# Optimization experiments

Measured on AMD Instinct MI355X. Metric: run time of the kernel, lower is better.

The kernel has to match this reference:

```python
import jax, jax.numpy as jnp
import numpy as np

N_NODES = 100000
D_FEAT = 64
E1 = 1600000  # 1-hop edges (avg degree 16)
E2 = 6400000  # 2-hop edges (avg degree 64)


def setup_inputs() -> dict:
    key = jax.random.key(0)
    k_x, k_ei1, k_w1, k_ei2, k_w2 = jax.random.split(key, 5)
    x = jax.random.normal(k_x, (N_NODES, D_FEAT), dtype=jnp.float32)
    edge_index1 = jax.random.randint(k_ei1, (2, E1), 0, N_NODES, dtype=jnp.int32)
    edge_weight1 = jax.random.uniform(k_w1, (E1,), dtype=jnp.float32)
    edge_index2 = jax.random.randint(k_ei2, (2, E2), 0, N_NODES, dtype=jnp.int32)
    edge_weight2 = jax.random.uniform(k_w2, (E2,), dtype=jnp.float32)
    return {
        "x": x,
        "edge_index1": edge_index1,
        "edge_weight1": edge_weight1,
        "edge_index2": edge_index2,
        "edge_weight2": edge_weight2,
    }


def _spmm(edge_index, edge_weight, x, num_nodes):
    # out[i] = sum_{(i,j) in E} w_ij * x[j]   (COO SpMM via gather + segment_sum)
    dst, src = edge_index[0], edge_index[1]
    msgs = edge_weight[:, None] * x[src]            # [E, d] gather + scale
    return jax.ops.segment_sum(msgs, dst, num_segments=num_nodes)  # [N, d]


def reference(x, edge_index1, edge_weight1, edge_index2, edge_weight2):
    n = x.shape[0]
    x1 = _spmm(edge_index1, edge_weight1, x, n)  # adj_t @ x
    x2 = _spmm(edge_index2, edge_weight2, x, n)  # adj_t2 @ x
    return jnp.concatenate([x1, x2], axis=1)     # [N, 2d]
```

## Files before the change

### kernel.cpp

```cpp
#include <hip/hip_runtime.h>
#include <hip/hip_bf16.h>

#define D 64
#define RB 8
#define RSZ 256
#define MAXB 1024
#define CH 4096
#define SCT 1024
#define GCH 4096

__global__ __launch_bounds__(256) void spmm_atomic_kernel(
    const int* __restrict__ idx, const float* __restrict__ wgt,
    const float* __restrict__ x, float* __restrict__ out, int E, int col_off) {
    const int lane   = threadIdx.x & 63;
    const int wave   = (blockIdx.x * blockDim.x + threadIdx.x) >> 6;
    const int nwaves = (gridDim.x * blockDim.x) >> 6;
    const int chunk = (E + nwaves - 1) / nwaves;
    int e0 = wave * chunk, e1 = min(e0 + chunk, E);
    for (int e = e0; e < e1; ++e) {
        const int dst = idx[e], src = idx[E + e];
        const float v = wgt[e] * x[src * D + lane];
        atomicAdd(&out[dst * 2 * D + col_off + lane], v);
    }
}

__global__ __launch_bounds__(256) void cvt_kernel(
    const float* __restrict__ x, unsigned short* __restrict__ xb, int total4) {
    int i = blockIdx.x * blockDim.x + threadIdx.x;
    if (i >= total4) return;
    float4 v = ((const float4*)x)[i];
    ushort4 o;
    unsigned u;
    u = __float_as_uint(v.x); o.x = (unsigned short)((u + 0x7FFF + ((u >> 16) & 1)) >> 16);
    u = __float_as_uint(v.y); o.y = (unsigned short)((u + 0x7FFF + ((u >> 16) & 1)) >> 16);
    u = __float_as_uint(v.z); o.z = (unsigned short)((u + 0x7FFF + ((u >> 16) & 1)) >> 16);
    u = __float_as_uint(v.w); o.w = (unsigned short)((u + 0x7FFF + ((u >> 16) & 1)) >> 16);
    ((ushort4*)xb)[i] = o;
}

__device__ __forceinline__ void decode_edge(
    int e, const int* __restrict__ ei1, const float* __restrict__ ew1,
    const int* __restrict__ ei2, const float* __restrict__ ew2,
    int E1, int E2, int nranges, int& b, int& src, float& w, int& dl) {
    int dst;
    if (e < E1) { dst = ei1[e]; src = ei1[E1 + e]; w = ew1[e]; b = dst >> RB; }
    else { int f = e - E1; dst = ei2[f]; src = ei2[E2 + f]; w = ew2[f];
           b = nranges + (dst >> RB); }
    dl = dst & (RSZ - 1);
}

__global__ __launch_bounds__(256) void hist_kernel(
    const int* __restrict__ ei1, const int* __restrict__ ei2,
    int E1, int E2, int nranges, int nbc, int* __restrict__ counts) {
    __shared__ int lhist[MAXB];
    const int t = threadIdx.x;
    for (int i = t; i < nbc; i += 256) lhist[i] = 0;
    __syncthreads();
    const int Etot = E1 + E2;
    for (int e = blockIdx.x * 256 + t; e < Etot; e += gridDim.x * 256) {
        int b = (e < E1) ? (ei1[e] >> RB) : (nranges + (ei2[e - E1] >> RB));
        atomicAdd(&lhist[b], 1);
    }
    __syncthreads();
    for (int i = t; i < nbc; i += 256)
        if (lhist[i]) atomicAdd(&counts[i], lhist[i]);
}

__global__ __launch_bounds__(1024) void scan_kernel(
    const int* __restrict__ counts, int nbc,
    int* __restrict__ starts, int* __restrict__ cursor) {
    __shared__ int lds[1024];
    const int t = threadIdx.x;
    int v = (t < nbc) ? counts[t] : 0;
    lds[t] = v;
    __syncthreads();
    for (int off = 1; off < 1024; off <<= 1) {
        int add = (t >= off) ? lds[t - off] : 0;
        __syncthreads();
        lds[t] += add;
        __syncthreads();
    }
    if (t < nbc) { starts[t] = lds[t] - v; cursor[t] = lds[t] - v; }
    if (t == nbc - 1) starts[nbc] = lds[t];
}

__global__ __launch_bounds__(1024) void scatter_kernel(
    const int* __restrict__ ei1, const float* __restrict__ ew1,
    const int* __restrict__ ei2, const float* __restrict__ ew2,
    int E1, int E2, int nranges, int nbc,
    int* __restrict__ cursor, int2* __restrict__ entries) {
    __shared__ int lstart[MAXB];
    __shared__ int lcur[MAXB];
    __shared__ int gbase[MAXB];
    __shared__ int2 ebuf[CH];
    __shared__ unsigned short ebkt[CH];

    const int t = threadIdx.x;
    const int Etot = E1 + E2;
    const int c0 = blockIdx.x * CH;
    const int cnt = min(CH, Etot - c0);

    int   eb[4], epk[4];
    float ewt[4];
#pragma unroll
    for (int i = 0; i < 4; ++i) {
        const int idx = t + i * SCT;
        eb[i] = 0; epk[i] = 0; ewt[i] = 0.f;
        if (idx < cnt) {
            int b, src, dl; float w;
            decode_edge(c0 + idx, ei1, ew1, ei2, ew2, E1, E2, nranges, b, src, w, dl);
            eb[i]  = b;
            epk[i] = src | (dl << 17);
            ewt[i] = w;
        }
    }

    for (int i = t; i < nbc; i += SCT) lcur[i] = 0;
    __syncthreads();
#pragma unroll
    for (int i = 0; i < 4; ++i) {
        const int idx = t + i * SCT;
        if (idx < cnt) atomicAdd(&lcur[eb[i]], 1);
    }
    __syncthreads();
    int v = (t < nbc) ? lcur[t] : 0;
    lstart[t] = v;
    __syncthreads();
    for (int off = 1; off < SCT; off <<= 1) {
        int add = (t >= off) ? lstart[t - off] : 0;
        __syncthreads();
        lstart[t] += add;
        __syncthreads();
    }
    int ex = lstart[t] - v;
    __syncthreads();
    if (t < nbc) {
        lstart[t] = ex;
        lcur[t]   = ex;
        gbase[t]  = v ? atomicAdd(&cursor[t], v) : 0;
    }
    __syncthreads();
#pragma unroll
    for (int i = 0; i < 4; ++i) {
        const int idx = t + i * SCT;
        if (idx < cnt) {
            int pos = atomicAdd(&lcur[eb[i]], 1);
            ebuf[pos] = make_int2(epk[i], __float_as_int(ewt[i]));
            ebkt[pos] = (unsigned short)eb[i];
        }
    }
    __syncthreads();
    for (int i = t; i < cnt; i += SCT) {
        int b = ebkt[i];
        entries[gbase[b] + (i - lstart[b])] = ebuf[i];
    }
}

__global__ __launch_bounds__(1024, 8) void gather_kernel(
    const int2* __restrict__ entries, const int* __restrict__ starts,
    const unsigned short* __restrict__ xb, float* __restrict__ out,
    int N, int nranges) {
    __shared__ int2 sbuf[GCH];
    __shared__ int shist[RSZ];
    __shared__ int sstart[RSZ];
    __shared__ int scur[RSZ];

    const int t    = threadIdx.x;
    const int lane = t & 63;
    const int wv   = t >> 6;
    const int c    = (blockIdx.x < nranges) ? (nranges + blockIdx.x)
                                            : (blockIdx.x - nranges);
    const int hop  = (c >= nranges) ? 1 : 0;
    const int r0   = (c - hop * nranges) << RB;

    const int s = starts[c];
    const int e = starts[c + 1];

    float acc[16];
#pragma unroll
    for (int i = 0; i < 16; ++i) acc[i] = 0.f;

    for (int cb = s; cb < e; cb += GCH) {
        const int cnt = min(GCH, e - cb);
        if (t < RSZ) shist[t] = 0;
        __syncthreads();

        int2 ent[4];
#pragma unroll
        for (int i = 0; i < 4; ++i) {
            const int idx = t + i * 1024;
            if (idx < cnt) {
                ent[i] = entries[cb + idx];
                atomicAdd(&shist[(ent[i].x >> 17) & (RSZ - 1)], 1);
            }
        }
        __syncthreads();

        if (t < RSZ) sstart[t] = shist[t];
        __syncthreads();
        for (int off = 1; off < RSZ; off <<= 1) {
            int v = 0;
            if (t < RSZ && t >= off) v = sstart[t - off];
            __syncthreads();
            if (t < RSZ) sstart[t] += v;
            __syncthreads();
        }
        if (t < RSZ) { int ex = sstart[t] - shist[t]; sstart[t] = ex; scur[t] = ex; }
        __syncthreads();

#pragma unroll
        for (int i = 0; i < 4; ++i) {
            const int idx = t + i * 1024;
            if (idx < cnt) {
                int pos = atomicAdd(&scur[(ent[i].x >> 17) & (RSZ - 1)], 1);
                sbuf[pos] = ent[i];
            }
        }
        __syncthreads();

#pragma unroll
        for (int nl = 0; nl < 16; ++nl) {
            const int dl = (wv << 4) + nl;
            const int js = sstart[dl];
            const int je = js + shist[dl];
            float a = acc[nl];
#pragma unroll 4
            for (int j = js; j < je; ++j) {
                const int2 q  = sbuf[j];
                const float w = __int_as_float(q.y);
                const int src = q.x & 0x1FFFF;
                const unsigned xv = xb[src * D + lane];
                a += w * __uint_as_float(xv << 16);
            }
            acc[nl] = a;
        }
        __syncthreads();
    }

#pragma unroll
    for (int nl = 0; nl < 16; ++nl) {
        const int node = r0 + (wv << 4) + nl;
        if (node < N) out[node * 2 * D + hop * D + lane] = acc[nl];
    }
}

extern "C" void kernel_launch(void* const* d_in, const int* in_sizes, int n_in,
                              void* d_out, int out_size, void* d_ws, size_t ws_size,
                              hipStream_t stream) {
    const float* x   = (const float*)d_in[0];
    const int*   ei1 = (const int*)d_in[1];
    const float* ew1 = (const float*)d_in[2];
    const int*   ei2 = (const int*)d_in[3];
    const float* ew2 = (const float*)d_in[4];

    const int E1 = in_sizes[2];
    const int E2 = in_sizes[4];
    const int N  = in_sizes[0] / D;
    const int Etot = E1 + E2;
    const int nranges = (N + RSZ - 1) >> RB;
    const int nbc = 2 * nranges;

    float* out = (float*)d_out;

    size_t off_entries = 0;
    size_t off_xb      = off_entries + (size_t)Etot * sizeof(int2);
    size_t off_counts  = off_xb + (((size_t)N * D * sizeof(unsigned short) + 15) & ~15ull);
    size_t off_starts  = off_counts + (size_t)nbc * sizeof(int);
    size_t off_cursor  = off_starts + (size_t)(nbc + 1) * sizeof(int);
    size_t needed      = off_cursor + (size_t)nbc * sizeof(int);

    if (ws_size < needed || nbc > MAXB || N > (1 << 17) || (N * D) % 4 != 0) {
        hipMemsetAsync(d_out, 0, (size_t)out_size * sizeof(float), stream);
        spmm_atomic_kernel<<<2048, 256, 0, stream>>>(ei1, ew1, x, out, E1, 0);
        spmm_atomic_kernel<<<2048, 256, 0, stream>>>(ei2, ew2, x, out, E2, D);
        return;
    }

    char* ws = (char*)d_ws;
    int2*           entries = (int2*)(ws + off_entries);
    unsigned short* xbuf    = (unsigned short*)(ws + off_xb);
    int*            counts  = (int*)(ws + off_counts);
    int*            starts  = (int*)(ws + off_starts);
    int*            cursor  = (int*)(ws + off_cursor);

    hipMemsetAsync(counts, 0, (size_t)nbc * sizeof(int), stream);

    const int total4 = (N * D) / 4;
    cvt_kernel<<<(total4 + 255) / 256, 256, 0, stream>>>(x, xbuf, total4);
    hist_kernel<<<1024, 256, 0, stream>>>(ei1, ei2, E1, E2, nranges, nbc, counts);
    scan_kernel<<<1, 1024, 0, stream>>>(counts, nbc, starts, cursor);
    const int nchunks = (Etot + CH - 1) / CH;
    scatter_kernel<<<nchunks, SCT, 0, stream>>>(ei1, ew1, ei2, ew2, E1, E2,
                                                nranges, nbc, cursor, entries);
    gather_kernel<<<nbc, 1024, 0, stream>>>(entries, starts, xbuf, out, N, nranges);
}
```

Baseline: 326.4 us.

## Fuse bf16 convert with histogram and process two edges per wave in gather

Merges the bf16 conversion and the bucket histogram kernels into one launch by splitting the grid's blocks between the two jobs, which removes a launch and lets both run concurrently. In the gather kernel each half-wave now handles a different edge, and each lane loads two bf16 features as one 32-bit word. This halves the serial edge-loop iterations per destination node and widens each load. The two halves are combined with a cross-lane shuffle, and the output is written as float2. The cost is extra registers for the doubled accumulators and a masked tail when a node has an odd edge count.

```diff
diff --git a/kernel.cpp b/kernel.cpp
--- a/kernel.cpp
+++ b/kernel.cpp
@@ -24,18 +24,39 @@
     }
 }
 
-__global__ __launch_bounds__(256) void cvt_kernel(
-    const float* __restrict__ x, unsigned short* __restrict__ xb, int total4) {
-    int i = blockIdx.x * blockDim.x + threadIdx.x;
-    if (i >= total4) return;
-    float4 v = ((const float4*)x)[i];
-    ushort4 o;
-    unsigned u;
-    u = __float_as_uint(v.x); o.x = (unsigned short)((u + 0x7FFF + ((u >> 16) & 1)) >> 16);
-    u = __float_as_uint(v.y); o.y = (unsigned short)((u + 0x7FFF + ((u >> 16) & 1)) >> 16);
-    u = __float_as_uint(v.z); o.z = (unsigned short)((u + 0x7FFF + ((u >> 16) & 1)) >> 16);
-    u = __float_as_uint(v.w); o.w = (unsigned short)((u + 0x7FFF + ((u >> 16) & 1)) >> 16);
-    ((ushort4*)xb)[i] = o;
+__global__ __launch_bounds__(256) void prep_kernel(
+    const float* __restrict__ x, unsigned short* __restrict__ xb, int total4,
+    const int* __restrict__ ei1, const int* __restrict__ ei2,
+    int E1, int E2, int nranges, int nbc, int* __restrict__ counts,
+    int cvtBlocks) {
+    __shared__ int lhist[MAXB];
+    if ((int)blockIdx.x < cvtBlocks) {
+        int i = blockIdx.x * 256 + threadIdx.x;
+        if (i < total4) {
+            float4 v = ((const float4*)x)[i];
+            ushort4 o;
+            unsigned u;
+            u = __float_as_uint(v.x); o.x = (unsigned short)((u + 0x7FFF + ((u >> 16) & 1)) >> 16);
+            u = __float_as_uint(v.y); o.y = (unsigned short)((u + 0x7FFF + ((u >> 16) & 1)) >> 16);
+            u = __float_as_uint(v.z); o.z = (unsigned short)((u + 0x7FFF + ((u >> 16) & 1)) >> 16);
+            u = __float_as_uint(v.w); o.w = (unsigned short)((u + 0x7FFF + ((u >> 16) & 1)) >> 16);
+            ((ushort4*)xb)[i] = o;
+        }
+        return;
+    }
+    const int hb = blockIdx.x - cvtBlocks;
+    const int nhb = gridDim.x - cvtBlocks;
+    const int t = threadIdx.x;
+    for (int i = t; i < nbc; i += 256) lhist[i] = 0;
+    __syncthreads();
+    const int Etot = E1 + E2;
+    for (int e = hb * 256 + t; e < Etot; e += nhb * 256) {
+        int b = (e < E1) ? (ei1[e] >> RB) : (nranges + (ei2[e - E1] >> RB));
+        atomicAdd(&lhist[b], 1);
+    }
+    __syncthreads();
+    for (int i = t; i < nbc; i += 256)
+        if (lhist[i]) atomicAdd(&counts[i], lhist[i]);
 }
 
 __device__ __forceinline__ void decode_edge(
@@ -47,23 +68,6 @@
     else { int f = e - E1; dst = ei2[f]; src = ei2[E2 + f]; w = ew2[f];
            b = nranges + (dst >> RB); }
     dl = dst & (RSZ - 1);
-}
-
-__global__ __launch_bounds__(256) void hist_kernel(
-    const int* __restrict__ ei1, const int* __restrict__ ei2,
-    int E1, int E2, int nranges, int nbc, int* __restrict__ counts) {
-    __shared__ int lhist[MAXB];
-    const int t = threadIdx.x;
-    for (int i = t; i < nbc; i += 256) lhist[i] = 0;
-    __syncthreads();
-    const int Etot = E1 + E2;
-    for (int e = blockIdx.x * 256 + t; e < Etot; e += gridDim.x * 256) {
-        int b = (e < E1) ? (ei1[e] >> RB) : (nranges + (ei2[e - E1] >> RB));
-        atomicAdd(&lhist[b], 1);
-    }
-    __syncthreads();
-    for (int i = t; i < nbc; i += 256)
-        if (lhist[i]) atomicAdd(&counts[i], lhist[i]);
 }
 
 __global__ __launch_bounds__(1024) void scan_kernel(
@@ -167,6 +171,8 @@
 
     const int t    = threadIdx.x;
     const int lane = t & 63;
+    const int half = lane >> 5;
+    const int fl   = lane & 31;
     const int wv   = t >> 6;
     const int c    = (blockIdx.x < nranges) ? (nranges + blockIdx.x)
                                             : (blockIdx.x - nranges);
@@ -176,9 +182,9 @@
     const int s = starts[c];
     const int e = starts[c + 1];
 
-    float acc[16];
-#pragma unroll
-    for (int i = 0; i < 16; ++i) acc[i] = 0.f;
+    float accx[16], accy[16];
+#pragma unroll
+    for (int i = 0; i < 16; ++i) { accx[i] = 0.f; accy[i] = 0.f; }
 
     for (int cb = s; cb < e; cb += GCH) {
         const int cnt = min(GCH, e - cb);
@@ -223,24 +229,33 @@
             const int dl = (wv << 4) + nl;
             const int js = sstart[dl];
             const int je = js + shist[dl];
-            float a = acc[nl];
+            float ax = accx[nl], ay = accy[nl];
 #pragma unroll 4
-            for (int j = js; j < je; ++j) {
-                const int2 q  = sbuf[j];
-                const float w = __int_as_float(q.y);
+            for (int j = js; j < je; j += 2) {
+                const int jj = j + half;
+                const bool ok = (jj < je);
+                const int jr = ok ? jj : j;
+                const int2 q = sbuf[jr];
+                float w = __int_as_float(q.y);
+                if (!ok) w = 0.f;
                 const int src = q.x & 0x1FFFF;
-                const unsigned xv = xb[src * D + lane];
-                a += w * __uint_as_float(xv << 16);
+                const unsigned u = *(const unsigned*)(xb + src * D + fl * 2);
+                ax += w * __uint_as_float(u << 16);
+                ay += w * __uint_as_float(u & 0xFFFF0000u);
             }
-            acc[nl] = a;
+            accx[nl] = ax; accy[nl] = ay;
         }
         __syncthreads();
     }
 
 #pragma unroll
     for (int nl = 0; nl < 16; ++nl) {
+        const float ax = accx[nl] + __shfl_xor(accx[nl], 32);
+        const float ay = accy[nl] + __shfl_xor(accy[nl], 32);
         const int node = r0 + (wv << 4) + nl;
-        if (node < N) out[node * 2 * D + hop * D + lane] = acc[nl];
+        if (half == 0 && node < N) {
+            ((float2*)(out + node * 2 * D + hop * D))[fl] = make_float2(ax, ay);
+        }
     }
 }
 
@@ -286,8 +301,9 @@
     hipMemsetAsync(counts, 0, (size_t)nbc * sizeof(int), stream);
 
     const int total4 = (N * D) / 4;
-    cvt_kernel<<<(total4 + 255) / 256, 256, 0, stream>>>(x, xbuf, total4);
-    hist_kernel<<<1024, 256, 0, stream>>>(ei1, ei2, E1, E2, nranges, nbc, counts);
+    const int cvtBlocks = (total4 + 255) / 256;
+    prep_kernel<<<cvtBlocks + 1024, 256, 0, stream>>>(
+        x, xbuf, total4, ei1, ei2, E1, E2, nranges, nbc, counts, cvtBlocks);
     scan_kernel<<<1, 1024, 0, stream>>>(counts, nbc, starts, cursor);
     const int nchunks = (Etot + CH - 1) / CH;
     scatter_kernel<<<nchunks, SCT, 0, stream>>>(ei1, ew1, ei2, ew2, E1, E2,
```

Result: slower. 408.7 us (+25.2%).
